# Performance work log

Hardware: AMD Instinct MI355X
Metric: run time of the kernel (lower is better)

Reference implementation:

```python
import jax, jax.numpy as jnp
import numpy as np

N, E, D = 20000, 160000, 128   # nodes, edges, d_model
GH, HC = 4, 128                # TransformerConv heads, per-head channels (= out_channels)
MH = 4                         # temporal MHA heads
MC = D // MH                   # temporal MHA per-head dim
EPS = 1e-5


def layer_norm(x, g, b):
    mu = x.mean(-1, keepdims=True)
    var = ((x - mu) ** 2).mean(-1, keepdims=True)
    return (x - mu) * jax.lax.rsqrt(var + EPS) * g + b


def forward(x, temporal_encoding, gq_w, gq_b, gk_w, gk_b, gv_w, gv_b, gs_w, gs_b,
            mha_wq, mha_bq, mha_wk, mha_bk, mha_wv, mha_bv, mha_wo, mha_bo,
            ffn_w1, ffn_b1, ffn_w2, ffn_b2,
            ln1_g, ln1_b, ln2_g, ln2_b, ln3_g, ln3_b, edge_index):
    src, dst = edge_index[0], edge_index[1]
    n = x.shape[0]
    # --- TransformerConv(in=D, out=D, heads=GH, concat=False, root_weight=True) ---
    q = (x @ gq_w.T + gq_b).reshape(n, GH, HC)
    k = (x @ gk_w.T + gk_b).reshape(n, GH, HC)
    v = (x @ gv_w.T + gv_b).reshape(n, GH, HC)
    # per-edge attention logits: <q_i, k_j> / sqrt(out_channels), message j->i
    alpha = (q[dst] * k[src]).sum(-1) / jnp.sqrt(jnp.asarray(HC, x.dtype))  # [E, GH]
    # numerically-stable segment softmax over incoming edges of each dst node
    m = jax.ops.segment_max(alpha, dst, num_segments=n)                     # [N, GH]
    ex = jnp.exp(alpha - m[dst])
    den = jax.ops.segment_sum(ex, dst, num_segments=n)
    w = ex / den[dst]                                                       # [E, GH]
    agg = jax.ops.segment_sum(w[..., None] * v[src], dst, num_segments=n)  # [N, GH, HC]
    graph_out = agg.mean(1) + (x @ gs_w.T + gs_b)  # concat=False -> head mean; + root skip lin
    x1 = layer_norm(x + graph_out, ln1_g, ln1_b)   # dropout is identity at eval
    # --- temporal MHA: per-node query (len 1) attends to its temporal encoding (kv len 1) ---
    tq = (x1 @ mha_wq.T + mha_bq).reshape(n, MH, MC)
    tk = (temporal_encoding @ mha_wk.T + mha_bk).reshape(n, MH, MC)
    tv = (temporal_encoding @ mha_wv.T + mha_bv).reshape(n, MH, MC)
    scores = (tq * tk).sum(-1, keepdims=True) / jnp.sqrt(jnp.asarray(MC, x.dtype))  # [N, MH, 1]
    attn = jax.nn.softmax(scores, axis=-1)  # exactly ones (single kv position); kept for fidelity
    temp_out = (attn * tv).reshape(n, D) @ mha_wo.T + mha_bo
    x2 = layer_norm(x1 + temp_out, ln2_g, ln2_b)
    # --- FFN ---
    h = jax.nn.relu(x2 @ ffn_w1.T + ffn_b1)
    ffn_out = h @ ffn_w2.T + ffn_b2
    return layer_norm(x2 + ffn_out, ln3_g, ln3_b)


def setup_inputs() -> dict:
    ks = jax.random.split(jax.random.key(0), 16)
    s = 0.05
    def p(i, shape):
        return jax.random.normal(ks[i], shape, jnp.float32) * s
    z = lambda *sh: jnp.zeros(sh, jnp.float32)
    o = lambda *sh: jnp.ones(sh, jnp.float32)
    return {
        "x": p(0, (N, D)),
        "temporal_encoding": p(1, (N, D)),
        "gq_w": p(2, (GH * HC, D)), "gq_b": z(GH * HC),
        "gk_w": p(3, (GH * HC, D)), "gk_b": z(GH * HC),
        "gv_w": p(4, (GH * HC, D)), "gv_b": z(GH * HC),
        "gs_w": p(5, (D, D)), "gs_b": z(D),
        "mha_wq": p(6, (D, D)), "mha_bq": z(D),
        "mha_wk": p(7, (D, D)), "mha_bk": z(D),
        "mha_wv": p(8, (D, D)), "mha_bv": z(D),
        "mha_wo": p(9, (D, D)), "mha_bo": z(D),
        "ffn_w1": p(10, (4 * D, D)), "ffn_b1": z(4 * D),
        "ffn_w2": p(11, (D, 4 * D)), "ffn_b2": z(D),
        "ln1_g": o(D), "ln1_b": z(D),
        "ln2_g": o(D), "ln2_b": z(D),
        "ln3_g": o(D), "ln3_b": z(D),
        "edge_index": jax.random.randint(ks[12], (2, E), 0, N, jnp.int32),
    }


def reference(x, temporal_encoding, gq_w, gq_b, gk_w, gk_b, gv_w, gv_b, gs_w, gs_b,
              mha_wq, mha_bq, mha_wk, mha_bk, mha_wv, mha_bv, mha_wo, mha_bo,
              ffn_w1, ffn_b1, ffn_w2, ffn_b2,
              ln1_g, ln1_b, ln2_g, ln2_b, ln3_g, ln3_b, edge_index):
    return forward(x, temporal_encoding, gq_w, gq_b, gk_w, gk_b, gv_w, gv_b, gs_w, gs_b,
                   mha_wq, mha_bq, mha_wk, mha_bk, mha_wv, mha_bv, mha_wo, mha_bo,
                   ffn_w1, ffn_b1, ffn_w2, ffn_b2,
                   ln1_g, ln1_b, ln2_g, ln2_b, ln3_g, ln3_b, edge_index)
```

## Files before the change

### kernel.cpp

```cpp
#include <hip/hip_runtime.h>

#define NN 20000
#define EE 160000
#define DD 128
#define GHC 512
#define INV_SQRT_HC 0.08838834764831845f

typedef __attribute__((ext_vector_type(8))) short short8;
typedef __attribute__((ext_vector_type(4))) short short4v;
typedef __attribute__((ext_vector_type(4))) float float4v;
typedef __attribute__((ext_vector_type(2))) float float2v;
typedef __attribute__((ext_vector_type(4))) unsigned uint4v;
typedef __attribute__((ext_vector_type(2))) unsigned uint2v;

__device__ inline float bf2f(unsigned short u) {
    union { unsigned u; float f; } x; x.u = ((unsigned)u) << 16; return x.f;
}
__device__ inline unsigned short f2bf(float f) {
    union { float f; unsigned u; } x; x.f = f;
    unsigned u = x.u;
    unsigned r = (u + 0x7fffu + ((u >> 16) & 1u)) >> 16;
    return (unsigned short)r;
}

#if defined(__has_builtin)
#if __has_builtin(__builtin_amdgcn_cvt_pk_f32_fp8) && __has_builtin(__builtin_amdgcn_cvt_pk_fp8_f32)
#define HW_FP8 1
#endif
#endif
#ifndef HW_FP8
#define HW_FP8 0
#endif

#if !HW_FP8
__device__ inline unsigned char sw_enc_fp8(float f) {
    if (!(f == f)) return 0x7f;
    unsigned s = (f < 0.f) ? 0x80u : 0u;
    float a = fabsf(f);
    if (a >= 448.f) return (unsigned char)(s | 0x7e);
    if (a < 5.96046448e-8f) return (unsigned char)s;
    int e; frexpf(a, &e);
    int E = e - 1;
    if (E < -6) E = -6;
    float q = ldexpf(rintf(ldexpf(a, 3 - E)), E - 3);
    if (q == 0.f) return (unsigned char)s;
    union { float f; unsigned u; } x; x.f = q;
    int qe = (int)((x.u >> 23) & 0xff) - 127;
    if (qe < -6) {
        unsigned mant = (unsigned)rintf(ldexpf(q, 9));
        return (unsigned char)(s | mant);
    }
    unsigned mant = (x.u >> 20) & 7;
    int ebits = qe + 7;
    if (ebits > 15) { ebits = 15; mant = 6; }
    return (unsigned char)(s | ((unsigned)ebits << 3) | mant);
}
__device__ inline float sw_dec_fp8(unsigned char u) {
    unsigned s = u >> 7, e = (u >> 3) & 15, m = u & 7;
    float v = e ? ldexpf((float)(8 + m), (int)e - 10) : ldexpf((float)m, -9);
    return s ? -v : v;
}
#endif

__device__ inline unsigned short fp8_enc2(float a, float b) {
#if HW_FP8
    int r = __builtin_amdgcn_cvt_pk_fp8_f32(a, b, 0, false);
    return (unsigned short)(r & 0xffff);
#else
    return (unsigned short)(sw_enc_fp8(a) | ((unsigned)sw_enc_fp8(b) << 8));
#endif
}
__device__ inline float2v fp8_dec2_lo(unsigned w) {
#if HW_FP8
    return __builtin_amdgcn_cvt_pk_f32_fp8((int)w, false);
#else
    float2v r;
    r[0] = sw_dec_fp8((unsigned char)(w & 0xff));
    r[1] = sw_dec_fp8((unsigned char)((w >> 8) & 0xff));
    return r;
#endif
}
__device__ inline float2v fp8_dec2_hi(unsigned w) {
#if HW_FP8
    return __builtin_amdgcn_cvt_pk_f32_fp8((int)w, true);
#else
    float2v r;
    r[0] = sw_dec_fp8((unsigned char)((w >> 16) & 0xff));
    r[1] = sw_dec_fp8((unsigned char)(w >> 24));
    return r;
#endif
}

struct WPack { const void* in[18]; };
__device__ __constant__ const int WSZ[18] = {
    65536, 65536, 65536, 512, 512, 512,
    16384, 128, 65536, 512, 65536, 128,
    128, 128, 128, 128, 128, 128 };

__global__ void prep_kernel(const float* __restrict__ x, const float* __restrict__ te,
                            unsigned short* __restrict__ xcout, WPack p,
                            unsigned short* __restrict__ wcout,
                            const float* __restrict__ wv, const float* __restrict__ bv,
                            const float* __restrict__ wo, const float* __restrict__ bo,
                            unsigned short* __restrict__ wcomb,
                            unsigned short* __restrict__ bcomb,
                            const int* __restrict__ e_dst, int* __restrict__ counts)
{
    const int b = blockIdx.x;
    const int tid = threadIdx.x;
    if (b < 1024) {
        const long n4half = (long)NN * DD / 4;
        short4v* out4 = reinterpret_cast<short4v*>(xcout);
        long i = (long)b * 256 + tid;
        const long stride = 1024L * 256;
        const long tot = 2 * n4half;
        for (; i < tot; i += stride) {
            const float4v* src = (i < n4half)
                ? reinterpret_cast<const float4v*>(x)
                : reinterpret_cast<const float4v*>(te) - n4half;
            float4v v = src[i];
            short4v o;
            o[0] = (short)f2bf(v[0]); o[1] = (short)f2bf(v[1]);
            o[2] = (short)f2bf(v[2]); o[3] = (short)f2bf(v[3]);
            out4[i] = o;
        }
    } else if (b < 1600) {
        const int seg = (b - 1024) >> 5;
        const int rep = (b - 1024) & 31;
        int off = 0;
#pragma unroll
        for (int s = 0; s < 18; ++s) if (s < seg) off += WSZ[s];
        const int n = WSZ[seg];
        const float* q = (const float*)p.in[seg];
        for (int i = rep * 256 + tid; i < n; i += 32 * 256)
            wcout[off + i] = f2bf(q[i]);
    } else if (b < 1664) {
        int e = (b - 1600) * 256 + tid;
        int i = e >> 7, kk = e & 127;
        float s = 0.f;
        for (int j = 0; j < 128; ++j)
            s += wo[i * 128 + j] * wv[j * 128 + kk];
        wcomb[e] = f2bf(s);
        if (b == 1600 && tid < 128) {
            float t = 0.f;
            for (int j = 0; j < 128; ++j) t += wo[tid * 128 + j] * bv[j];
            bcomb[tid] = f2bf(t + bo[tid]);
        }
    } else {
        int e = (b - 1664) * 256 + tid;
        if (e < EE) {
            int d = e_dst[e];
            if (d >= 0 && d < NN) atomicAdd(&counts[d], 1);
        }
    }
}

__global__ __launch_bounds__(256) void gemm3_kernel(
    const unsigned short* __restrict__ A, const unsigned short* __restrict__ W,
    const unsigned short* __restrict__ bias, unsigned short* __restrict__ out,
    unsigned char* __restrict__ kvout, int M, int Nout, int split, int relu)
{
    __shared__ short8 wslab[2048];
    __shared__ __attribute__((aligned(16))) unsigned stile[4][16][36];
    const int tid  = threadIdx.x;
    const int lane = tid & 63;
    const int wid  = tid >> 6;
    const int quad = lane >> 4;
    const int l15  = lane & 15;
    const int rowbase  = blockIdx.x * 64 + wid * 16;
    const int colbase0 = blockIdx.y * 128;
    const bool isfp8 = (colbase0 >= split);
    const int kvcol = colbase0 - split;
    const int which = isfp8 ? (kvcol >> 9) : 0;
    const int head  = isfp8 ? ((kvcol & 511) >> 7) : 0;

    const short8* A8 = reinterpret_cast<const short8*>(A);
    const short8* W8 = reinterpret_cast<const short8*>(W);

#pragma unroll
    for (int rep = 0; rep < 8; ++rep) {
        int f   = rep * 256 + tid;
        int fl  = f & 63;
        int fi  = (f >> 6) & 3;
        int ft  = (f >> 8) & 3;
        int ftt = f >> 10;
        int wrow = colbase0 + ftt * 64 + 16 * ft + (fl & 15);
        wslab[f] = W8[(size_t)wrow * 16 + fi * 4 + (fl >> 4)];
    }

    int arow = rowbase + l15;
    if (arow >= M) arow = M - 1;
    short8 a4[4];
#pragma unroll
    for (int i = 0; i < 4; ++i) a4[i] = A8[(size_t)arow * 16 + i * 4 + quad];

    __syncthreads();

    unsigned short* fp = reinterpret_cast<unsigned short*>(&stile[wid][0][0]);

#pragma unroll
    for (int tt = 0; tt < 2; ++tt) {
        const int colbase = colbase0 + tt * 64;
        float4v acc[4];
#pragma unroll
        for (int t = 0; t < 4; ++t) acc[t] = (float4v){0.f, 0.f, 0.f, 0.f};

#pragma unroll
        for (int i = 0; i < 4; ++i) {
#pragma unroll
            for (int t = 0; t < 4; ++t) {
                short8 b = wslab[((tt * 4 + t) * 4 + i) * 64 + lane];
                acc[t] = __builtin_amdgcn_mfma_f32_16x16x32_bf16(a4[i], b, acc[t], 0, 0, 0);
            }
        }

        if (!isfp8) {
#pragma unroll
            for (int t = 0; t < 4; ++t) {
                float bv = bf2f(bias[colbase + 16 * t + l15]);
#pragma unroll
                for (int r = 0; r < 4; ++r) {
                    float vv = acc[t][r] + bv;
                    if (relu) vv = fmaxf(vv, 0.f);
                    float ov = __shfl_xor(vv, 1, 64);
                    if ((l15 & 1) == 0)
                        stile[wid][quad * 4 + r][8 * t + (l15 >> 1)] =
                            (unsigned)f2bf(vv) | ((unsigned)f2bf(ov) << 16);
                }
            }
            const int rr0 = lane >> 3;
            const int cd  = (lane & 7) * 4;
#pragma unroll
            for (int it = 0; it < 2; ++it) {
                int rr = rr0 + it * 8;
                int grow = rowbase + rr;
                if (grow < M) {
                    uint4v v = *reinterpret_cast<const uint4v*>(&stile[wid][rr][cd]);
                    *reinterpret_cast<uint4v*>(&out[(size_t)grow * Nout + colbase0 + tt * 64 + cd * 2]) = v;
                }
            }
        } else {
#pragma unroll
            for (int t = 0; t < 4; ++t) {
                float bv = bf2f(bias[colbase + 16 * t + l15]);
#pragma unroll
                for (int r = 0; r < 4; ++r) {
                    float vv = (acc[t][r] + bv) * 256.f;
                    float ov = __shfl_xor(vv, 1, 64);
                    if ((l15 & 1) == 0)
                        fp[(quad * 4 + r) * 72 + tt * 32 + ((16 * t + l15) >> 1)] =
                            fp8_enc2(vv, ov);
                }
            }
        }
    }

    if (isfp8) {
#pragma unroll
        for (int it = 0; it < 2; ++it) {
            int u = lane + it * 64;
            int row = u >> 3;
            int part = u & 7;
            int grow = rowbase + row;
            if (grow < M) {
                uint4v v = *reinterpret_cast<const uint4v*>(&fp[row * 72 + part * 8]);
                size_t ro = (size_t)grow * 1024 + (size_t)which * 512
                          + (size_t)head * 128 + (size_t)part * 16;
                *reinterpret_cast<uint4v*>(kvout + ro) = v;
            }
        }
    }
}

__global__ __launch_bounds__(256) void gemm_ln2_kernel(
    const unsigned short* __restrict__ A, const unsigned short* __restrict__ W,
    const unsigned short* __restrict__ bias,
    const float* __restrict__ residf, const float* __restrict__ c,
    const unsigned short* __restrict__ g, const unsigned short* __restrict__ beta,
    float* __restrict__ outf, unsigned short* __restrict__ outb, int M, int K)
{
    __shared__ short8 wslab[2048];
    __shared__ unsigned short stile[4][16][136];
    const int tid  = threadIdx.x;
    const int lane = tid & 63;
    const int wid  = tid >> 6;
    const int quad = lane >> 4;
    const int l15  = lane & 15;
    const int rowbase = blockIdx.x * 64 + wid * 16;

    int arow = rowbase + l15;
    if (arow >= M) arow = M - 1;

    const short8* A8 = reinterpret_cast<const short8*>(A);
    const short8* W8 = reinterpret_cast<const short8*>(W);
    const int k8 = K >> 3;
    const int kchunks = K >> 7;

    float4v acc[2][4];
#pragma unroll
    for (int tt = 0; tt < 2; ++tt)
#pragma unroll
        for (int t = 0; t < 4; ++t) acc[tt][t] = (float4v){0.f, 0.f, 0.f, 0.f};

    for (int cc = 0; cc < kchunks; ++cc) {
        if (cc > 0) __syncthreads();
#pragma unroll
        for (int rep = 0; rep < 8; ++rep) {
            int f   = rep * 256 + tid;
            int fl  = f & 63;
            int fi  = (f >> 6) & 3;
            int ft  = (f >> 8) & 3;
            int ftt = f >> 10;
            int wrow = ftt * 64 + 16 * ft + (fl & 15);
            wslab[f] = W8[(size_t)wrow * k8 + cc * 16 + fi * 4 + (fl >> 4)];
        }
        short8 a4[4];
#pragma unroll
        for (int i = 0; i < 4; ++i) a4[i] = A8[(size_t)arow * k8 + cc * 16 + i * 4 + quad];
        __syncthreads();
#pragma unroll
        for (int tt = 0; tt < 2; ++tt)
#pragma unroll
            for (int i = 0; i < 4; ++i)
#pragma unroll
                for (int t = 0; t < 4; ++t) {
                    short8 b = wslab[((tt * 4 + t) * 4 + i) * 64 + lane];
                    acc[tt][t] = __builtin_amdgcn_mfma_f32_16x16x32_bf16(a4[i], b, acc[tt][t], 0, 0, 0);
                }
    }

#pragma unroll
    for (int tt = 0; tt < 2; ++tt)
#pragma unroll
        for (int t = 0; t < 4; ++t) {
            float bv = bf2f(bias[tt * 64 + 16 * t + l15]);
#pragma unroll
            for (int r = 0; r < 4; ++r)
                stile[wid][quad * 4 + r][tt * 64 + 16 * t + l15] = f2bf(acc[tt][t][r] + bv);
        }

    const int r  = lane >> 2;
    const int p  = lane & 3;
    const int grow = rowbase + r;
    const int gr = (grow < M) ? grow : M - 1;

    float v[32];
    const short8* st8 = reinterpret_cast<const short8*>(&stile[wid][r][p * 32]);
#pragma unroll
    for (int q = 0; q < 4; ++q) {
        short8 sb = st8[q];
#pragma unroll
        for (int j = 0; j < 8; ++j) v[q * 8 + j] = bf2f((unsigned short)sb[j]);
    }
    const float4v* r4 = reinterpret_cast<const float4v*>(&residf[(size_t)gr * 128 + p * 32]);
#pragma unroll
    for (int q = 0; q < 8; ++q) {
        float4v rv = r4[q];
#pragma unroll
        for (int j = 0; j < 4; ++j) v[q * 4 + j] += rv[j];
    }
    if (c) {
        const float4v* c4 = reinterpret_cast<const float4v*>(&c[(size_t)gr * 128 + p * 32]);
#pragma unroll
        for (int q = 0; q < 8; ++q) {
            float4v cv = c4[q];
#pragma unroll
            for (int j = 0; j < 4; ++j) v[q * 4 + j] += cv[j];
        }
    }
    float s = 0.f, sq = 0.f;
#pragma unroll
    for (int i = 0; i < 32; ++i) { s += v[i]; sq += v[i] * v[i]; }
    s  += __shfl_xor(s, 1, 64);  s  += __shfl_xor(s, 2, 64);
    sq += __shfl_xor(sq, 1, 64); sq += __shfl_xor(sq, 2, 64);
    float mu  = s * (1.f / 128.f);
    float var = sq * (1.f / 128.f) - mu * mu;
    float rs  = rsqrtf(fmaxf(var, 0.f) + 1e-5f);

    if (grow < M) {
        const short8* g8 = reinterpret_cast<const short8*>(&g[p * 32]);
        const short8* b8 = reinterpret_cast<const short8*>(&beta[p * 32]);
        float o[32];
#pragma unroll
        for (int q = 0; q < 4; ++q) {
            short8 gg = g8[q], bb = b8[q];
#pragma unroll
            for (int j = 0; j < 8; ++j)
                o[q * 8 + j] = (v[q * 8 + j] - mu) * rs * bf2f((unsigned short)gg[j])
                               + bf2f((unsigned short)bb[j]);
        }
        float4v* o4 = reinterpret_cast<float4v*>(outf + (size_t)grow * 128 + p * 32);
#pragma unroll
        for (int q = 0; q < 8; ++q) {
            float4v ov = {o[q * 4], o[q * 4 + 1], o[q * 4 + 2], o[q * 4 + 3]};
            o4[q] = ov;
        }
        if (outb) {
            short8* ob8 = reinterpret_cast<short8*>(outb + (size_t)grow * 128 + p * 32);
#pragma unroll
            for (int q = 0; q < 4; ++q) {
                short8 oo;
#pragma unroll
                for (int j = 0; j < 8; ++j) oo[j] = (short)f2bf(o[q * 8 + j]);
                ob8[q] = oo;
            }
        }
    }
}

__global__ __launch_bounds__(1024) void scan_kernel(
    const int* __restrict__ counts, int* __restrict__ offsets, int* __restrict__ pos, int n)
{
    __shared__ int wsum[16];
    __shared__ int carry_s;
    const int tid = threadIdx.x;
    const int wid = tid >> 6, lane = tid & 63;
    int vals[20];
#pragma unroll
    for (int cI = 0; cI < 20; ++cI) {
        int i = cI * 1024 + tid;
        vals[cI] = (i < n) ? counts[i] : 0;
    }
    if (tid == 0) carry_s = 0;
    __syncthreads();
#pragma unroll
    for (int cI = 0; cI < 20; ++cI) {
        int i = cI * 1024 + tid;
        int val = vals[cI];
        int x = val;
#pragma unroll
        for (int off = 1; off < 64; off <<= 1) {
            int t = __shfl_up(x, off, 64);
            if (lane >= off) x += t;
        }
        if (lane == 63) wsum[wid] = x;
        __syncthreads();
        if (wid == 0 && lane < 16) {
            int s = wsum[lane];
#pragma unroll
            for (int off = 1; off < 16; off <<= 1) {
                int t = __shfl_up(s, off, 64);
                if (lane >= off) s += t;
            }
            wsum[lane] = s;
        }
        __syncthreads();
        int prefix = (wid > 0 ? wsum[wid - 1] : 0) + carry_s;
        int ex = prefix + x - val;
        if (i < n) { offsets[i] = ex; pos[i] = ex; }
        __syncthreads();
        if (tid == 0) carry_s += wsum[15];
        __syncthreads();
    }
    if (tid == 0) offsets[n] = carry_s;
}

__global__ void scatter_kernel(const int* __restrict__ src, const int* __restrict__ dst,
                               int* __restrict__ pos, int* __restrict__ sorted_src, int E)
{
    int e = blockIdx.x * 256 + threadIdx.x;
    if (e < E) {
        int d = dst[e];
        if (d >= 0 && d < NN) {
            int p = atomicAdd(&pos[d], 1);
            if (p >= 0 && p < E) sorted_src[p] = src[e];
        }
    }
}

__device__ inline void agg_edge(const uint2v& kk, const uint2v& vv,
                                const float* qf, float* acc, float& ssum)
{
    float2v k01 = fp8_dec2_lo(kk[0]);
    float2v k23 = fp8_dec2_hi(kk[0]);
    float2v k45 = fp8_dec2_lo(kk[1]);
    float2v k67 = fp8_dec2_hi(kk[1]);
    float dot = qf[0] * k01[0] + qf[1] * k01[1] + qf[2] * k23[0] + qf[3] * k23[1]
              + qf[4] * k45[0] + qf[5] * k45[1] + qf[6] * k67[0] + qf[7] * k67[1];
    dot += __shfl_xor(dot, 1, 64);
    dot += __shfl_xor(dot, 2, 64);
    dot += __shfl_xor(dot, 4, 64);
    dot += __shfl_xor(dot, 8, 64);
    float pp = __expf(dot);
    ssum += pp;
    float2v v01 = fp8_dec2_lo(vv[0]);
    float2v v23 = fp8_dec2_hi(vv[0]);
    float2v v45 = fp8_dec2_lo(vv[1]);
    float2v v67 = fp8_dec2_hi(vv[1]);
    acc[0] += pp * v01[0]; acc[1] += pp * v01[1];
    acc[2] += pp * v23[0]; acc[3] += pp * v23[1];
    acc[4] += pp * v45[0]; acc[5] += pp * v45[1];
    acc[6] += pp * v67[0]; acc[7] += pp * v67[1];
}

__global__ __launch_bounds__(256) void agg_kernel(
    const unsigned short* __restrict__ q, const unsigned char* __restrict__ kvb,
    const int* __restrict__ offsets, const int* __restrict__ srcs,
    float* __restrict__ aggb)
{
    __shared__ float sacc[4][64][8];
    __shared__ float sssum[4][64];
    const int tid  = threadIdx.x;
    const int wid  = tid >> 6;
    const int lane = tid & 63;
    const int node = blockIdx.x * 2 + (wid >> 1);
    const int half = wid & 1;

    const short8* q8 = reinterpret_cast<const short8*>(q);
    const int fidx = (lane >> 4) * 16 + (lane & 15);
    const int koff = fidx * 8;

    short8 qv = q8[(size_t)node * 64 + fidx];
    float qf[8];
#pragma unroll
    for (int i = 0; i < 8; ++i)
        qf[i] = bf2f((unsigned short)qv[i]) * (INV_SQRT_HC / 256.f);

    int beg = offsets[node], end = offsets[node + 1];
    if (beg < 0) beg = 0;
    if (end > EE) end = EE;
    float ssum = 0.f;
    float acc[8];
#pragma unroll
    for (int i = 0; i < 8; ++i) acc[i] = 0.f;

    const int start = beg + half;
    int nce = (end > start) ? ((end - start + 1) >> 1) : 0;
    int ncap = (nce > 64) ? 64 : nce;

    int sv = 0;
    if (lane < ncap) {
        int s = srcs[start + 2 * lane];
        if (s < 0) s = 0;
        if (s >= NN) s = NN - 1;
        sv = s;
    }
    if (ncap > 0) {
        int s0 = __shfl(sv, 0, 64);
        uint2v kc = *reinterpret_cast<const uint2v*>(kvb + (size_t)s0 * 1024 + koff);
        uint2v vc = *reinterpret_cast<const uint2v*>(kvb + (size_t)s0 * 1024 + 512 + koff);
        for (int i = 0; i < ncap; ++i) {
            uint2v kn, vn;
            if (i + 1 < ncap) {
                int sn = __shfl(sv, i + 1, 64);
                kn = *reinterpret_cast<const uint2v*>(kvb + (size_t)sn * 1024 + koff);
                vn = *reinterpret_cast<const uint2v*>(kvb + (size_t)sn * 1024 + 512 + koff);
            }
            agg_edge(kc, vc, qf, acc, ssum);
            kc = kn; vc = vn;
        }
    }
    for (int j = start + 128; j < end; j += 2) {
        int s = srcs[j];
        if (s < 0) s = 0;
        if (s >= NN) s = NN - 1;
        uint2v kc = *reinterpret_cast<const uint2v*>(kvb + (size_t)s * 1024 + koff);
        uint2v vc = *reinterpret_cast<const uint2v*>(kvb + (size_t)s * 1024 + 512 + koff);
        agg_edge(kc, vc, qf, acc, ssum);
    }

#pragma unroll
    for (int i = 0; i < 8; ++i) sacc[wid][lane][i] = acc[i];
    sssum[wid][lane] = ssum;
    __syncthreads();
    if (half == 0) {
#pragma unroll
        for (int i = 0; i < 8; ++i) acc[i] += sacc[wid ^ 1][lane][i];
        ssum += sssum[wid ^ 1][lane];

        float inv = (ssum > 0.f) ? 1.f / (256.f * ssum) : 0.f;
#pragma unroll
        for (int i = 0; i < 8; ++i) acc[i] *= inv;
#pragma unroll
        for (int i = 0; i < 8; ++i) {
            acc[i] += __shfl_xor(acc[i], 16, 64);
            acc[i] += __shfl_xor(acc[i], 32, 64);
            acc[i] *= 0.25f;
        }
        if (lane < 16) {
            float4v* o = reinterpret_cast<float4v*>(aggb + (size_t)node * 128 + lane * 8);
            o[0] = (float4v){acc[0], acc[1], acc[2], acc[3]};
            o[1] = (float4v){acc[4], acc[5], acc[6], acc[7]};
        }
    }
}

extern "C" void kernel_launch(void* const* d_in, const int* in_sizes, int n_in,
                              void* d_out, int out_size, void* d_ws, size_t ws_size,
                              hipStream_t stream)
{
    const int* edge_index = (const int*)d_in[28];
    const int* e_src = edge_index;
    const int* e_dst = edge_index + EE;

    if (n_in < 29 || in_sizes[0] != NN * DD || in_sizes[28] != 2 * EE || out_size != NN * DD)
        return;

    const size_t SZ_OFF  = (size_t)(NN + 16) * 4;
    const size_t SZ_CNT  = (size_t)NN * 4;
    const size_t SZ_SS   = (size_t)EE * 4;
    const size_t SZ_SM   = (size_t)NN * DD * 2;
    const size_t SZ_F32  = (size_t)NN * DD * 4;
    const size_t SZ_Q    = (size_t)NN * 512 * 2;
    const size_t SZ_KV   = (size_t)NN * 1024;
    const size_t SZ_HB   = (size_t)NN * GHC * 2;
    const size_t WC_ELE  = 347136;
    const size_t SZ_WC   = WC_ELE * 2;
    const size_t SZ_WCB  = 16384 * 2 + 256;
    const size_t REQUIRED = SZ_OFF + 2 * SZ_CNT + SZ_SS + 2 * SZ_SM + SZ_WC + SZ_WCB
                          + SZ_Q + SZ_KV + 3 * SZ_F32 + SZ_SM + SZ_HB;

    if (ws_size < REQUIRED) return;

    char* w = (char*)d_ws;
    int* offsets = (int*)w;        w += SZ_OFF;
    int* counts  = (int*)w;        w += SZ_CNT;
    int* pos     = (int*)w;        w += SZ_CNT;
    int* sorted_src = (int*)w;     w += SZ_SS;
    unsigned short* xc   = (unsigned short*)w; w += SZ_SM;
    unsigned short* tec  = (unsigned short*)w; w += SZ_SM;
    unsigned short* wc   = (unsigned short*)w; w += SZ_WC;
    unsigned short* wcomb = (unsigned short*)w; w += 16384 * 2;
    unsigned short* bcomb = (unsigned short*)w; w += 256;
    unsigned short* qb   = (unsigned short*)w; w += SZ_Q;
    unsigned char*  kvb  = (unsigned char*)w;  w += SZ_KV;
    float*          aggb = (float*)w;          w += SZ_F32;
    float*          x1f  = (float*)w;          w += SZ_F32;
    float*          x2f  = (float*)w;          w += SZ_F32;
    unsigned short* x2b  = (unsigned short*)w; w += SZ_SM;
    unsigned short* hbuf = (unsigned short*)w; w += SZ_HB;

    unsigned short* cw = wc;
    unsigned short* qkv_w = cw; cw += 3 * 65536;
    unsigned short* qkv_b = cw; cw += 3 * 512;
    unsigned short* gs_w  = cw; cw += 16384;  unsigned short* gs_b  = cw; cw += 128;
    unsigned short* ffn_w1 = cw; cw += 65536; unsigned short* ffn_b1 = cw; cw += 512;
    unsigned short* ffn_w2 = cw; cw += 65536; unsigned short* ffn_b2 = cw; cw += 128;
    unsigned short* ln1_g = cw; cw += 128;    unsigned short* ln1_b = cw; cw += 128;
    unsigned short* ln2_g = cw; cw += 128;    unsigned short* ln2_b = cw; cw += 128;
    unsigned short* ln3_g = cw; cw += 128;    unsigned short* ln3_b = cw; cw += 128;

    const int EB = (EE + 255) / 256;
    const dim3 blk(256);
    const int MB = (NN + 63) / 64;

    WPack pack;
    const int live_idx[18] = {2,4,6, 3,5,7, 8,9, 18,19, 20,21, 22,23,24,25,26,27};
    for (int i = 0; i < 18; ++i) pack.in[i] = d_in[live_idx[i]];

    (void)hipMemsetAsync(counts, 0, SZ_CNT, stream);
    prep_kernel<<<1664 + EB, blk, 0, stream>>>((const float*)d_in[0], (const float*)d_in[1],
                                               xc, pack, wc,
                                               (const float*)d_in[14], (const float*)d_in[15],
                                               (const float*)d_in[16], (const float*)d_in[17],
                                               wcomb, bcomb, e_dst, counts);

    scan_kernel<<<1, 1024, 0, stream>>>(counts, offsets, pos, NN);
    scatter_kernel<<<EB, blk, 0, stream>>>(e_src, e_dst, pos, sorted_src, EE);

    gemm3_kernel<<<dim3(MB, 12), blk, 0, stream>>>(xc, qkv_w, qkv_b, qb, kvb,
                                                   NN, 512, 512, 0);
    agg_kernel<<<NN / 2, blk, 0, stream>>>(qb, kvb, offsets, sorted_src, aggb);
    gemm_ln2_kernel<<<MB, blk, 0, stream>>>(xc, gs_w, gs_b, (const float*)d_in[0], aggb,
                                            ln1_g, ln1_b, x1f, nullptr, NN, DD);
    gemm_ln2_kernel<<<MB, blk, 0, stream>>>(tec, wcomb, bcomb, x1f, nullptr,
                                            ln2_g, ln2_b, x2f, x2b, NN, DD);
    gemm3_kernel<<<dim3(MB, 4), blk, 0, stream>>>(x2b, ffn_w1, ffn_b1, hbuf, nullptr,
                                                  NN, 512, 99999, 1);
    gemm_ln2_kernel<<<MB, blk, 0, stream>>>(hbuf, ffn_w2, ffn_b2, x2f, nullptr,
                                            ln3_g, ln3_b, (float*)d_out, nullptr, NN, GHC);
}
```

Measured before the change: 291.5 us.

## Loop each GEMM block over four row tiles, prefetch A, swizzle blocks to XCDs

```diff
diff --git a/kernel.cpp b/kernel.cpp
--- a/kernel.cpp
+++ b/kernel.cpp
@@ -158,7 +158,8 @@
 __global__ __launch_bounds__(256) void gemm3_kernel(
     const unsigned short* __restrict__ A, const unsigned short* __restrict__ W,
     const unsigned short* __restrict__ bias, unsigned short* __restrict__ out,
-    unsigned char* __restrict__ kvout, int M, int Nout, int split, int relu)
+    unsigned char* __restrict__ kvout, int M, int Nout, int split, int relu,
+    int nxg, int ncol)
 {
     __shared__ short8 wslab[2048];
     __shared__ __attribute__((aligned(16))) unsigned stile[4][16][36];
@@ -167,8 +168,17 @@
     const int wid  = tid >> 6;
     const int quad = lane >> 4;
     const int l15  = lane & 15;
-    const int rowbase  = blockIdx.x * 64 + wid * 16;
-    const int colbase0 = blockIdx.y * 128;
+
+    const int nb  = nxg * ncol;
+    const int qq  = nb >> 3, rm = nb & 7;
+    const int xcd = blockIdx.x & 7, slot = blockIdx.x >> 3;
+    const int c   = (xcd < rm) ? xcd * (qq + 1) + slot
+                               : rm * (qq + 1) + (xcd - rm) * qq + slot;
+    const int xg = c / ncol;
+    const int yg = c - xg * ncol;
+    const int colbase0 = yg * 128;
+    const int rowg = xg * 256;
+
     const bool isfp8 = (colbase0 >= split);
     const int kvcol = colbase0 - split;
     const int which = isfp8 ? (kvcol >> 9) : 0;
@@ -176,6 +186,14 @@
 
     const short8* A8 = reinterpret_cast<const short8*>(A);
     const short8* W8 = reinterpret_cast<const short8*>(W);
+
+    short8 a4[4];
+    {
+        int arow = rowg + wid * 16 + l15;
+        if (arow >= M) arow = M - 1;
+#pragma unroll
+        for (int i = 0; i < 4; ++i) a4[i] = A8[(size_t)arow * 16 + i * 4 + quad];
+    }
 
 #pragma unroll
     for (int rep = 0; rep < 8; ++rep) {
@@ -188,86 +206,102 @@
         wslab[f] = W8[(size_t)wrow * 16 + fi * 4 + (fl >> 4)];
     }
 
-    int arow = rowbase + l15;
-    if (arow >= M) arow = M - 1;
-    short8 a4[4];
-#pragma unroll
-    for (int i = 0; i < 4; ++i) a4[i] = A8[(size_t)arow * 16 + i * 4 + quad];
+    float bvv[2][4];
+#pragma unroll
+    for (int tt = 0; tt < 2; ++tt)
+#pragma unroll
+        for (int t = 0; t < 4; ++t)
+            bvv[tt][t] = bf2f(bias[colbase0 + tt * 64 + 16 * t + l15]);
 
     __syncthreads();
 
     unsigned short* fp = reinterpret_cast<unsigned short*>(&stile[wid][0][0]);
 
 #pragma unroll
-    for (int tt = 0; tt < 2; ++tt) {
-        const int colbase = colbase0 + tt * 64;
-        float4v acc[4];
-#pragma unroll
-        for (int t = 0; t < 4; ++t) acc[t] = (float4v){0.f, 0.f, 0.f, 0.f};
-
-#pragma unroll
-        for (int i = 0; i < 4; ++i) {
-#pragma unroll
-            for (int t = 0; t < 4; ++t) {
-                short8 b = wslab[((tt * 4 + t) * 4 + i) * 64 + lane];
-                acc[t] = __builtin_amdgcn_mfma_f32_16x16x32_bf16(a4[i], b, acc[t], 0, 0, 0);
-            }
-        }
-
-        if (!isfp8) {
-#pragma unroll
-            for (int t = 0; t < 4; ++t) {
-                float bv = bf2f(bias[colbase + 16 * t + l15]);
-#pragma unroll
-                for (int r = 0; r < 4; ++r) {
-                    float vv = acc[t][r] + bv;
-                    if (relu) vv = fmaxf(vv, 0.f);
-                    float ov = __shfl_xor(vv, 1, 64);
-                    if ((l15 & 1) == 0)
-                        stile[wid][quad * 4 + r][8 * t + (l15 >> 1)] =
-                            (unsigned)f2bf(vv) | ((unsigned)f2bf(ov) << 16);
+    for (int tg = 0; tg < 4; ++tg) {
+        const int rowbase = rowg + tg * 64 + wid * 16;
+
+        short8 a4n[4];
+        if (tg < 3) {
+            int arow = rowbase + 64 + l15;
+            if (arow >= M) arow = M - 1;
+#pragma unroll
+            for (int i = 0; i < 4; ++i) a4n[i] = A8[(size_t)arow * 16 + i * 4 + quad];
+        }
+
+#pragma unroll
+        for (int tt = 0; tt < 2; ++tt) {
+            float4v acc[4];
+#pragma unroll
+            for (int t = 0; t < 4; ++t) acc[t] = (float4v){0.f, 0.f, 0.f, 0.f};
+
+#pragma unroll
+            for (int i = 0; i < 4; ++i) {
+#pragma unroll
+                for (int t = 0; t < 4; ++t) {
+                    short8 b = wslab[((tt * 4 + t) * 4 + i) * 64 + lane];
+                    acc[t] = __builtin_amdgcn_mfma_f32_16x16x32_bf16(a4[i], b, acc[t], 0, 0, 0);
                 }
             }
-            const int rr0 = lane >> 3;
-            const int cd  = (lane & 7) * 4;
-#pragma unroll
-            for (int it = 0; it < 2; ++it) {
-                int rr = rr0 + it * 8;
-                int grow = rowbase + rr;
-                if (grow < M) {
-                    uint4v v = *reinterpret_cast<const uint4v*>(&stile[wid][rr][cd]);
-                    *reinterpret_cast<uint4v*>(&out[(size_t)grow * Nout + colbase0 + tt * 64 + cd * 2]) = v;
+
+            if (!isfp8) {
+#pragma unroll
+                for (int t = 0; t < 4; ++t) {
+#pragma unroll
+                    for (int r = 0; r < 4; ++r) {
+                        float vv = acc[t][r] + bvv[tt][t];
+                        if (relu) vv = fmaxf(vv, 0.f);
+                        float ov = __shfl_xor(vv, 1, 64);
+                        if ((l15 & 1) == 0)
+                            stile[wid][quad * 4 + r][8 * t + (l15 >> 1)] =
+                                (unsigned)f2bf(vv) | ((unsigned)f2bf(ov) << 16);
+                    }
+                }
+                const int rr0 = lane >> 3;
+                const int cd  = (lane & 7) * 4;
+#pragma unroll
+                for (int it = 0; it < 2; ++it) {
+                    int rw = rr0 + it * 8;
+                    int grow = rowbase + rw;
+                    if (grow < M) {
+                        uint4v v = *reinterpret_cast<const uint4v*>(&stile[wid][rw][cd]);
+                        *reinterpret_cast<uint4v*>(&out[(size_t)grow * Nout + colbase0 + tt * 64 + cd * 2]) = v;
+                    }
+                }
+            } else {
+#pragma unroll
+                for (int t = 0; t < 4; ++t) {
+#pragma unroll
+                    for (int r = 0; r < 4; ++r) {
+                        float vv = (acc[t][r] + bvv[tt][t]) * 256.f;
+                        float ov = __shfl_xor(vv, 1, 64);
+                        if ((l15 & 1) == 0)
+                            fp[(quad * 4 + r) * 72 + tt * 32 + ((16 * t + l15) >> 1)] =
+                                fp8_enc2(vv, ov);
+                    }
                 }
             }
-        } else {
-#pragma unroll
-            for (int t = 0; t < 4; ++t) {
-                float bv = bf2f(bias[colbase + 16 * t + l15]);
-#pragma unroll
-                for (int r = 0; r < 4; ++r) {
-                    float vv = (acc[t][r] + bv) * 256.f;
-                    float ov = __shfl_xor(vv, 1, 64);
-                    if ((l15 & 1) == 0)
-                        fp[(quad * 4 + r) * 72 + tt * 32 + ((16 * t + l15) >> 1)] =
-                            fp8_enc2(vv, ov);
+        }
+
+        if (isfp8) {
+#pragma unroll
+            for (int it = 0; it < 2; ++it) {
+                int u = lane + it * 64;
+                int row = u >> 3;
+                int part = u & 7;
+                int grow = rowbase + row;
+                if (grow < M) {
+                    uint4v v = *reinterpret_cast<const uint4v*>(&fp[row * 72 + part * 8]);
+                    size_t ro = (size_t)grow * 1024 + (size_t)which * 512
+                              + (size_t)head * 128 + (size_t)part * 16;
+                    *reinterpret_cast<uint4v*>(kvout + ro) = v;
                 }
             }
         }
-    }
-
-    if (isfp8) {
-#pragma unroll
-        for (int it = 0; it < 2; ++it) {
-            int u = lane + it * 64;
-            int row = u >> 3;
-            int part = u & 7;
-            int grow = rowbase + row;
-            if (grow < M) {
-                uint4v v = *reinterpret_cast<const uint4v*>(&fp[row * 72 + part * 8]);
-                size_t ro = (size_t)grow * 1024 + (size_t)which * 512
-                          + (size_t)head * 128 + (size_t)part * 16;
-                *reinterpret_cast<uint4v*>(kvout + ro) = v;
-            }
+
+        if (tg < 3) {
+#pragma unroll
+            for (int i = 0; i < 4; ++i) a4[i] = a4n[i];
         }
     }
 }
@@ -643,6 +677,7 @@
     const int EB = (EE + 255) / 256;
     const dim3 blk(256);
     const int MB = (NN + 63) / 64;
+    const int MB2 = (NN + 255) / 256;
 
     WPack pack;
     const int live_idx[18] = {2,4,6, 3,5,7, 8,9, 18,19, 20,21, 22,23,24,25,26,27};
@@ -658,15 +693,15 @@
     scan_kernel<<<1, 1024, 0, stream>>>(counts, offsets, pos, NN);
     scatter_kernel<<<EB, blk, 0, stream>>>(e_src, e_dst, pos, sorted_src, EE);
 
-    gemm3_kernel<<<dim3(MB, 12), blk, 0, stream>>>(xc, qkv_w, qkv_b, qb, kvb,
-                                                   NN, 512, 512, 0);
+    gemm3_kernel<<<dim3(MB2 * 12), blk, 0, stream>>>(xc, qkv_w, qkv_b, qb, kvb,
+                                                     NN, 512, 512, 0, MB2, 12);
     agg_kernel<<<NN / 2, blk, 0, stream>>>(qb, kvb, offsets, sorted_src, aggb);
     gemm_ln2_kernel<<<MB, blk, 0, stream>>>(xc, gs_w, gs_b, (const float*)d_in[0], aggb,
                                             ln1_g, ln1_b, x1f, nullptr, NN, DD);
     gemm_ln2_kernel<<<MB, blk, 0, stream>>>(tec, wcomb, bcomb, x1f, nullptr,
                                             ln2_g, ln2_b, x2f, x2b, NN, DD);
-    gemm3_kernel<<<dim3(MB, 4), blk, 0, stream>>>(x2b, ffn_w1, ffn_b1, hbuf, nullptr,
-                                                  NN, 512, 99999, 1);
+    gemm3_kernel<<<dim3(MB2 * 4), blk, 0, stream>>>(x2b, ffn_w1, ffn_b1, hbuf, nullptr,
+                                                    NN, 512, 99999, 1, MB2, 4);
     gemm_ln2_kernel<<<MB, blk, 0, stream>>>(hbuf, ffn_w2, ffn_b2, x2f, nullptr,
                                             ln3_g, ln3_b, (float*)d_out, nullptr, NN, GHC);
 }
```

After: 289.1 us. Within noise of the previous version (-0.8%).
